# Performance work log

Measured on AMD Instinct MI355X. Metric: run time of the kernel, lower is better.

## Reference

```python
import jax, jax.numpy as jnp
import numpy as np

NH, NL, NP = 8, 4, 4  # heads, levels, points per head per level
SHAPES = [(100, 134), (50, 67), (25, 34), (13, 17)]  # (H, W) per level, strides 8/16/32/64


def rms_norm(x, w, eps=1e-6):
    return x * jax.lax.rsqrt(jnp.mean(x * x, axis=-1, keepdims=True) + eps) * w


def bilinear_sample(value_l, loc, H, W):
    """grid_sample(bilinear, zeros padding, align_corners=False) equivalent.
    value_l: (bs, nh, H*W, d); loc: (bs, Lq, nh, P, 2) normalized to [0,1].
    Returns (bs, Lq, nh, P, d)."""
    bs, Lq, nh, P, _ = loc.shape
    x = loc[..., 0] * W - 0.5
    y = loc[..., 1] * H - 0.5
    x0 = jnp.floor(x); y0 = jnp.floor(y)
    lx = x - x0; ly = y - y0
    x0i = x0.astype(jnp.int32); y0i = y0.astype(jnp.int32)
    out = None
    for dy, dx in ((0, 0), (0, 1), (1, 0), (1, 1)):
        wgt = (lx if dx else 1.0 - lx) * (ly if dy else 1.0 - ly)
        xi = x0i + dx; yi = y0i + dy
        valid = (xi >= 0) & (xi < W) & (yi >= 0) & (yi < H)
        idx = jnp.clip(yi, 0, H - 1) * W + jnp.clip(xi, 0, W - 1)  # (bs,Lq,nh,P)
        idx_t = idx.transpose(0, 2, 1, 3).reshape(bs, nh, Lq * P)
        g = jnp.take_along_axis(value_l, idx_t[..., None], axis=2)  # (bs,nh,Lq*P,d)
        g = g.reshape(bs, nh, Lq, P, -1).transpose(0, 2, 1, 3, 4)    # (bs,Lq,nh,P,d)
        term = g * (wgt * valid)[..., None]
        out = term if out is None else out + term
    return out


def _forward(query, query_pos, reference_points, norm_attn_w, Wv, bv, Woff, boff, Waw, baw, Wo, bo, ls_attn_g, norm_ffn_w, W1, b1, W2, b2, W3, b3, ls_ffn_g):
    bs, Lq, C = query.shape
    d = C // NH
    # --- pre-norm MSDeformAttn with identity=0 (LayerScale residual applied outside) ---
    normed = rms_norm(query, norm_attn_w)
    q = normed + query_pos  # query_pos only affects offsets/weights, not value
    value = (normed @ Wv.T + bv).reshape(bs, Lq, NH, d).transpose(0, 2, 1, 3)  # (bs,nh,Nv,d)
    off = (q @ Woff.T + boff).reshape(bs, Lq, NH, NL, NP, 2)
    aw = jax.nn.softmax((q @ Waw.T + baw).reshape(bs, Lq, NH, NL * NP), axis=-1)
    aw = aw.reshape(bs, Lq, NH, NL, NP)
    normalizer = jnp.array([[w, h] for (h, w) in SHAPES], dtype=query.dtype)  # (NL,2) = (W,H)
    loc = reference_points[:, :, None, :, None, :] + off / normalizer[None, None, None, :, None, :]
    out = jnp.zeros((bs, Lq, NH, d), query.dtype)
    start = 0
    for l, (H, W) in enumerate(SHAPES):
        v_l = jax.lax.dynamic_slice_in_dim(value, start, H * W, axis=2)
        samp = bilinear_sample(v_l, loc[:, :, :, l], H, W)  # (bs,Lq,nh,P,d)
        out = out + jnp.einsum('bqhpd,bqhp->bqhd', samp, aw[:, :, :, l])
        start += H * W
    attn_out = out.reshape(bs, Lq, C) @ Wo.T + bo
    x = query + ls_attn_g * attn_out
    # --- pre-norm SwiGLU FFN with LayerScale residual ---
    n2 = rms_norm(x, norm_ffn_w)
    h = jax.nn.silu(n2 @ W1.T + b1) * (n2 @ W2.T + b2)
    return x + ls_ffn_g * (h @ W3.T + b3)


def setup_inputs() -> dict:
    key = jax.random.key(0)
    ks = jax.random.split(key, 12)
    bs, C, dffn = 2, 256, 1024
    Lq = sum(h * w for h, w in SHAPES)  # 17821
    p = 0.02
    return {
        'query': jax.random.normal(ks[0], (bs, Lq, C), jnp.float32),
        'query_pos': jax.random.normal(ks[1], (bs, Lq, C), jnp.float32),
        'reference_points': jax.random.uniform(ks[2], (bs, Lq, NL, 2), jnp.float32),
        'spatial_shapes': jnp.array(SHAPES, jnp.int32),
        'level_start_index': jnp.array(np.cumsum([0] + [h * w for h, w in SHAPES])[:-1], jnp.int32),
        'norm_attn_w': jnp.ones((C,), jnp.float32),
        'Wv': jax.random.normal(ks[3], (C, C), jnp.float32) * p,
        'bv': jnp.zeros((C,), jnp.float32),
        'Woff': jax.random.normal(ks[4], (NH * NL * NP * 2, C), jnp.float32) * p,
        'boff': jax.random.uniform(ks[5], (NH * NL * NP * 2,), jnp.float32, -1.0, 1.0),
        'Waw': jax.random.normal(ks[6], (NH * NL * NP, C), jnp.float32) * p,
        'baw': jnp.zeros((NH * NL * NP,), jnp.float32),
        'Wo': jax.random.normal(ks[7], (C, C), jnp.float32) * p,
        'bo': jnp.zeros((C,), jnp.float32),
        'ls_attn_g': jnp.full((C,), 1e-4, jnp.float32),
        'norm_ffn_w': jnp.ones((C,), jnp.float32),
        'W1': jax.random.normal(ks[8], (dffn, C), jnp.float32) * p,
        'b1': jnp.zeros((dffn,), jnp.float32),
        'W2': jax.random.normal(ks[9], (dffn, C), jnp.float32) * p,
        'b2': jnp.zeros((dffn,), jnp.float32),
        'W3': jax.random.normal(ks[10], (C, dffn), jnp.float32) * p,
        'b3': jnp.zeros((C,), jnp.float32),
        'ls_ffn_g': jnp.full((C,), 1e-4, jnp.float32),
    }


def reference(query, query_pos, reference_points, spatial_shapes, level_start_index, norm_attn_w, Wv, bv, Woff, boff, Waw, baw, Wo, bo, ls_attn_g, norm_ffn_w, W1, b1, W2, b2, W3, b3, ls_ffn_g):
    del spatial_shapes, level_start_index  # static shapes baked into SHAPES
    return _forward(query, query_pos, reference_points, norm_attn_w, Wv, bv, Woff, boff, Waw, baw, Wo, bo, ls_attn_g, norm_ffn_w, W1, b1, W2, b2, W3, b3, ls_ffn_g)
```

## Files before the change

### kernel.cpp

```cpp
#include <hip/hip_runtime.h>
#include <hip/hip_bf16.h>
#include <cstddef>

#define LQ   17821
#define BS   2
#define MTOK (BS * LQ)
#define CDIM 256
#define NHD  8
#define DHEAD 32
#define DFFN 1024

typedef short bf16x4 __attribute__((ext_vector_type(4)));
typedef short bf16x8 __attribute__((ext_vector_type(8)));
typedef float f32x4  __attribute__((ext_vector_type(4)));
typedef float f32x2  __attribute__((ext_vector_type(2)));

__device__ __forceinline__ unsigned char fp8_enc(float f) {
#if __has_builtin(__builtin_amdgcn_cvt_pk_fp8_f32)
    return (unsigned char)(__builtin_amdgcn_cvt_pk_fp8_f32(f, f, 0, false) & 0xff);
#else
    unsigned s = (__float_as_uint(f) >> 31) << 7;
    float af = fabsf(f);
    if (af < 0.0078125f) return (unsigned char)s;
    af = fminf(af, 448.f);
    unsigned b = __float_as_uint(af);
    int e = (int)(b >> 23) - 127 + 7;
    unsigned m = (b >> 20) & 7;
    if (b & 0x80000) { m++; if (m == 8) { m = 0; e++; } }
    if (e < 1) return (unsigned char)s;
    if (e > 15) { e = 15; m = 6; }
    return (unsigned char)(s | ((unsigned)e << 3) | m);
#endif
}

__device__ __forceinline__ float fp8_dec_byte(unsigned x) {
    unsigned s = (x >> 7) & 1, e = (x >> 3) & 15, m = x & 7;
    float v = e ? __uint_as_float(((e + 120u) << 23) | (m << 20))
                : (float)m * 0.001953125f;
    return s ? -v : v;
}

template <bool HI>
__device__ __forceinline__ f32x2 fp8_dec2(unsigned d) {
#if __has_builtin(__builtin_amdgcn_cvt_pk_f32_fp8)
    return __builtin_amdgcn_cvt_pk_f32_fp8(d, HI);
#else
    f32x2 r;
    r[0] = fp8_dec_byte((d >> (HI ? 16 : 0)) & 0xff);
    r[1] = fp8_dec_byte((d >> (HI ? 24 : 8)) & 0xff);
    return r;
#endif
}

struct CastJobs {
    const float* src[7];
    __hip_bfloat16* dst[7];
    const float* colw[7];
    int n[7];
};

__global__ __launch_bounds__(256)
void cast_all(CastJobs j) {
    const int seg = blockIdx.y;
    const int i = blockIdx.x * 256 + threadIdx.x;
    if (i < j.n[seg]) {
        float v = j.src[seg][i];
        if (j.colw[seg]) v *= j.colw[seg][i & 255];
        j.dst[seg][i] = (__hip_bfloat16)v;
    }
}

__device__ __forceinline__ ushort bfpack(float f) {
    __hip_bfloat16 h = (__hip_bfloat16)f;
    return *(ushort*)&h;
}

template <bool ADD_POS>
__global__ __launch_bounds__(256)
void rmsnorm_kernel(const float* __restrict__ x, const float* __restrict__ pos,
                    const float* __restrict__ w,
                    __hip_bfloat16* __restrict__ outN, __hip_bfloat16* __restrict__ outQ) {
    const int tok = blockIdx.x * 4 + (threadIdx.x >> 6);
    if (tok >= MTOK) return;
    const int lane = threadIdx.x & 63;
    const size_t base = (size_t)tok * CDIM + lane * 4;
    const float4 v = *(const float4*)&x[base];
    float ss = v.x * v.x + v.y * v.y + v.z * v.z + v.w * v.w;
#pragma unroll
    for (int m = 1; m < 64; m <<= 1) ss += __shfl_xor(ss, m, 64);
    const float r = rsqrtf(ss * (1.0f / CDIM) + 1e-6f);
    const float4 wv = *(const float4*)&w[lane * 4];
    const float n0 = v.x * r * wv.x, n1 = v.y * r * wv.y;
    const float n2 = v.z * r * wv.z, n3 = v.w * r * wv.w;
    ushort4 o;
    o.x = bfpack(n0); o.y = bfpack(n1); o.z = bfpack(n2); o.w = bfpack(n3);
    *(ushort4*)&outN[base] = o;
    if (ADD_POS) {
        const float4 p = *(const float4*)&pos[base];
        ushort4 q;
        q.x = bfpack(n0 + p.x); q.y = bfpack(n1 + p.y);
        q.z = bfpack(n2 + p.z); q.w = bfpack(n3 + p.w);
        *(ushort4*)&outQ[base] = q;
    }
}

__global__ __launch_bounds__(256)
void rowrms_kernel(const __hip_bfloat16* __restrict__ x, float* __restrict__ r) {
    const int tok = blockIdx.x * 4 + (threadIdx.x >> 6);
    if (tok >= MTOK) return;
    const int lane = threadIdx.x & 63;
    const ushort4 u = *(const ushort4*)&x[(size_t)tok * CDIM + lane * 4];
    const float v0 = __uint_as_float((unsigned)u.x << 16);
    const float v1 = __uint_as_float((unsigned)u.y << 16);
    const float v2 = __uint_as_float((unsigned)u.z << 16);
    const float v3 = __uint_as_float((unsigned)u.w << 16);
    float ss = v0 * v0 + v1 * v1 + v2 * v2 + v3 * v3;
#pragma unroll
    for (int m = 1; m < 64; m <<= 1) ss += __shfl_xor(ss, m, 64);
    if (lane == 0) r[tok] = rsqrtf(ss * (1.0f / CDIM) + 1e-6f);
}

#define GBM 128
#define GBN 128

template <int MODE, int BKT, typename OUTT>
__global__ __launch_bounds__(256, 2)
void mfma_gemm(const __hip_bfloat16* __restrict__ A,
               const __hip_bfloat16* __restrict__ B1, const float* __restrict__ bias1,
               const float* __restrict__ bias2,
               const float* __restrict__ resid, const __hip_bfloat16* __restrict__ residb,
               const float* __restrict__ ls,
               OUTT* __restrict__ out, int M, int N, int K) {
    constexpr int LDKT = BKT + 8;
    constexpr int CH = BKT / 16;
    constexpr int CPR = BKT / 8;

    __shared__ short As[GBM * LDKT];
    __shared__ short Bs[GBN * LDKT];

    const int tid = threadIdx.x;
    const int m0 = blockIdx.x * GBM;
    const int n0 = blockIdx.y * GBN;
    const int wave = tid >> 6;
    const int lane = tid & 63;
    const int wm = (wave >> 1) * 64;
    const int wn = (wave & 1) * 64;
    const int fr = lane & 15;
    const int fq = lane >> 4;

    f32x4 acc[4][4] = {};

    int srow[CH], skc[CH];
#pragma unroll
    for (int cc = 0; cc < CH; ++cc) {
        const int g = tid + cc * 256;
        srow[cc] = g / CPR;
        skc[cc] = (g % CPR) * 8;
    }
    const uint4 zero4 = make_uint4(0, 0, 0, 0);

    uint4 ra[CH], rb[CH];
#pragma unroll
    for (int cc = 0; cc < CH; ++cc) {
        const int gm = m0 + srow[cc];
        ra[cc] = (gm < M) ? *(const uint4*)&A[(size_t)gm * K + skc[cc]] : zero4;
        rb[cc] = *(const uint4*)&B1[(size_t)(n0 + srow[cc]) * K + skc[cc]];
    }

    for (int k0 = 0; k0 < K; k0 += BKT) {
        __syncthreads();
#pragma unroll
        for (int cc = 0; cc < CH; ++cc) {
            short* pa = &As[srow[cc] * LDKT + skc[cc]];
            short* pb = &Bs[srow[cc] * LDKT + skc[cc]];
            union { uint4 u; bf16x4 h[2]; } cv;
            cv.u = ra[cc]; ((bf16x4*)pa)[0] = cv.h[0]; ((bf16x4*)pa)[1] = cv.h[1];
            cv.u = rb[cc]; ((bf16x4*)pb)[0] = cv.h[0]; ((bf16x4*)pb)[1] = cv.h[1];
        }
        __syncthreads();

        if (k0 + BKT < K) {
            const int kn = k0 + BKT;
#pragma unroll
            for (int cc = 0; cc < CH; ++cc) {
                const int gm = m0 + srow[cc];
                ra[cc] = (gm < M) ? *(const uint4*)&A[(size_t)gm * K + kn + skc[cc]] : zero4;
                rb[cc] = *(const uint4*)&B1[(size_t)(n0 + srow[cc]) * K + kn + skc[cc]];
            }
        }

#pragma unroll
        for (int kk = 0; kk < BKT; kk += 32) {
            const int kq = kk + fq * 8;
            bf16x8 af[4], bfr[4];
#pragma unroll
            for (int i = 0; i < 4; ++i)
                af[i] = *(const bf16x8*)&As[(wm + i * 16 + fr) * LDKT + kq];
#pragma unroll
            for (int j = 0; j < 4; ++j)
                bfr[j] = *(const bf16x8*)&Bs[(wn + j * 16 + fr) * LDKT + kq];
#pragma unroll
            for (int i = 0; i < 4; ++i)
#pragma unroll
                for (int j = 0; j < 4; ++j)
                    acc[i][j] = __builtin_amdgcn_mfma_f32_16x16x32_bf16(af[i], bfr[j], acc[i][j], 0, 0, 0);
        }
    }

#pragma unroll
    for (int i = 0; i < 4; ++i) {
#pragma unroll
        for (int r = 0; r < 4; ++r) {
            const int m = m0 + wm + i * 16 + fq * 4 + r;
            if (m >= M) continue;
#pragma unroll
            for (int j = 0; j < 4; ++j) {
                const int n = n0 + wn + j * 16 + fr;
                float v;
                if constexpr (MODE == 4)
                    v = acc[i][j][r] + ((n < 256) ? bias1[n] : bias2[n - 256]);
                else
                    v = acc[i][j][r] + bias1[n];
                if constexpr (MODE == 0 || MODE == 4) {
                    out[(size_t)m * N + n] = (OUTT)v;
                } else if constexpr (MODE == 1) {
                    const int b = (m >= LQ) ? 1 : 0;
                    const int qi = m - b * LQ;
                    const int h = n >> 5;
                    const int c = n & 31;
                    ((unsigned char*)out)[((size_t)(b * NHD + h) * LQ + qi) * DHEAD + c] = fp8_enc(v);
                } else if constexpr (MODE == 2) {
                    out[(size_t)m * N + n] =
                        (OUTT)(resid[(size_t)m * N + n] + ls[n] * v);
                } else {
                    const float rx = __uint_as_float(
                        (unsigned)(*(const ushort*)&residb[(size_t)m * N + n]) << 16);
                    out[(size_t)m * N + n] = (OUTT)(rx + ls[n] * v);
                }
            }
        }
    }
}

__global__ __launch_bounds__(256, 3)
void mfma_swiglu(const __hip_bfloat16* __restrict__ A,
                 const __hip_bfloat16* __restrict__ B1, const float* __restrict__ bias1,
                 const __hip_bfloat16* __restrict__ B2, const float* __restrict__ bias2,
                 const float* __restrict__ rrow,
                 __hip_bfloat16* __restrict__ out, int M) {
    constexpr int BKT = 32, LDKT = 40, K = CDIM, N = DFFN;
    __shared__ short As[128 * LDKT];
    __shared__ short Bs[64 * LDKT];
    __shared__ short Bs2[64 * LDKT];

    const int tid = threadIdx.x;
    const int m0 = blockIdx.x * 128;
    const int n0 = blockIdx.y * 64;
    const int wave = tid >> 6;
    const int lane = tid & 63;
    const int wm = (wave >> 1) * 64;
    const int wn = (wave & 1) * 32;
    const int fr = lane & 15;
    const int fq = lane >> 4;

    f32x4 acc[4][2] = {};
    f32x4 acc2[4][2] = {};

    const int arow = tid >> 2;
    const int akc = (tid & 3) * 8;
    const uint4 zero4 = make_uint4(0, 0, 0, 0);

    uint4 ra0, ra1, rb, rc;
    {
        const int gm0 = m0 + arow, gm1 = m0 + arow + 64;
        ra0 = (gm0 < M) ? *(const uint4*)&A[(size_t)gm0 * K + akc] : zero4;
        ra1 = (gm1 < M) ? *(const uint4*)&A[(size_t)gm1 * K + akc] : zero4;
        rb = *(const uint4*)&B1[(size_t)(n0 + arow) * K + akc];
        rc = *(const uint4*)&B2[(size_t)(n0 + arow) * K + akc];
    }

    for (int k0 = 0; k0 < K; k0 += BKT) {
        __syncthreads();
        {
            union { uint4 u; bf16x4 h[2]; } cv;
            short* pa0 = &As[arow * LDKT + akc];
            short* pa1 = &As[(arow + 64) * LDKT + akc];
            short* pb = &Bs[arow * LDKT + akc];
            short* pc = &Bs2[arow * LDKT + akc];
            cv.u = ra0; ((bf16x4*)pa0)[0] = cv.h[0]; ((bf16x4*)pa0)[1] = cv.h[1];
            cv.u = ra1; ((bf16x4*)pa1)[0] = cv.h[0]; ((bf16x4*)pa1)[1] = cv.h[1];
            cv.u = rb;  ((bf16x4*)pb)[0] = cv.h[0]; ((bf16x4*)pb)[1] = cv.h[1];
            cv.u = rc;  ((bf16x4*)pc)[0] = cv.h[0]; ((bf16x4*)pc)[1] = cv.h[1];
        }
        __syncthreads();

        if (k0 + BKT < K) {
            const int kn = k0 + BKT + akc;
            const int gm0 = m0 + arow, gm1 = m0 + arow + 64;
            ra0 = (gm0 < M) ? *(const uint4*)&A[(size_t)gm0 * K + kn] : zero4;
            ra1 = (gm1 < M) ? *(const uint4*)&A[(size_t)gm1 * K + kn] : zero4;
            rb = *(const uint4*)&B1[(size_t)(n0 + arow) * K + kn];
            rc = *(const uint4*)&B2[(size_t)(n0 + arow) * K + kn];
        }

        const int kq = fq * 8;
        bf16x8 af[4], bfr[2], bg[2];
#pragma unroll
        for (int i = 0; i < 4; ++i)
            af[i] = *(const bf16x8*)&As[(wm + i * 16 + fr) * LDKT + kq];
#pragma unroll
        for (int j = 0; j < 2; ++j) {
            bfr[j] = *(const bf16x8*)&Bs[(wn + j * 16 + fr) * LDKT + kq];
            bg[j] = *(const bf16x8*)&Bs2[(wn + j * 16 + fr) * LDKT + kq];
        }
#pragma unroll
        for (int i = 0; i < 4; ++i)
#pragma unroll
            for (int j = 0; j < 2; ++j) {
                acc[i][j] = __builtin_amdgcn_mfma_f32_16x16x32_bf16(af[i], bfr[j], acc[i][j], 0, 0, 0);
                acc2[i][j] = __builtin_amdgcn_mfma_f32_16x16x32_bf16(af[i], bg[j], acc2[i][j], 0, 0, 0);
            }
    }

#pragma unroll
    for (int i = 0; i < 4; ++i) {
#pragma unroll
        for (int r = 0; r < 4; ++r) {
            const int m = m0 + wm + i * 16 + fq * 4 + r;
            if (m >= M) continue;
            const float rm = rrow[m];
#pragma unroll
            for (int j = 0; j < 2; ++j) {
                const int n = n0 + wn + j * 16 + fr;
                const float v1 = acc[i][j][r] * rm + bias1[n];
                const float v2 = acc2[i][j][r] * rm + bias2[n];
                const float sig = 1.0f / (1.0f + expf(-v1));
                out[(size_t)m * N + n] = (__hip_bfloat16)(v1 * sig * v2);
            }
        }
    }
}

__global__ __launch_bounds__(256)
void sample_kernel(const unsigned char* __restrict__ value,
                   const ushort* __restrict__ proj,
                   const float* __restrict__ ref,
                   __hip_bfloat16* __restrict__ out) {
    __shared__ float wsm[4][NHD][16];
    __shared__ int2  sTap[4][64][9];

    const int tok0 = blockIdx.x * 4;
    const int t = threadIdx.x;

    if (t < 32) {
        const int tl = t >> 3, h = t & 7;
        const int row = tok0 + tl;
        if (row < MTOK) {
            const ushort* lg = &proj[(size_t)row * 384 + 256 + h * 16];
            float v[16];
            float mx = -3.4e38f;
#pragma unroll
            for (int i = 0; i < 16; ++i) {
                v[i] = __uint_as_float((unsigned)lg[i] << 16);
                mx = fmaxf(mx, v[i]);
            }
            float s = 0.f;
#pragma unroll
            for (int i = 0; i < 16; ++i) { v[i] = expf(v[i] - mx); s += v[i]; }
            const float inv = 1.0f / s;
#pragma unroll
            for (int i = 0; i < 16; ++i) wsm[tl][h][i] = v[i] * inv;
        }
    }
    __syncthreads();

#pragma unroll
    for (int e = t; e < 512; e += 256) {
        const int tl = e >> 7, hp = e & 127;
        const int row = tok0 + tl;
        if (row < MTOK) {
            const int h = hp >> 4, pt = hp & 15, lv = pt >> 2;
            const int Hs[4] = {100, 50, 25, 13};
            const int Ws[4] = {134, 67, 34, 17};
            const int stt[4] = {0, 13400, 16750, 17600};
            const int H = Hs[lv], W = Ws[lv];
            const float rx = ref[((size_t)row * 4 + lv) * 2 + 0];
            const float ry = ref[((size_t)row * 4 + lv) * 2 + 1];
            const float ox = __uint_as_float((unsigned)proj[(size_t)row * 384 + h * 32 + pt * 2 + 0] << 16);
            const float oy = __uint_as_float((unsigned)proj[(size_t)row * 384 + h * 32 + pt * 2 + 1] << 16);
            const float xf = rx * (float)W + ox - 0.5f;
            const float yf = ry * (float)H + oy - 0.5f;
            const float x0f = floorf(xf), y0f = floorf(yf);
            const float fx = xf - x0f, fy = yf - y0f;
            const int x0 = (int)x0f, y0 = (int)y0f;
            const float aw = wsm[tl][h][pt];
            const int b = (row >= LQ) ? 1 : 0;
            const int base = (b * NHD + h) * LQ + stt[lv];
#pragma unroll
            for (int tap = 0; tap < 4; ++tap) {
                const int dy = tap >> 1, dx = tap & 1;
                const int xi = x0 + dx, yi = y0 + dy;
                const bool valid = (xi >= 0) & (xi < W) & (yi >= 0) & (yi < H);
                const float wgt = (dx ? fx : 1.f - fx) * (dy ? fy : 1.f - fy) * aw;
                sTap[tl][pt * 4 + tap][h] = valid
                    ? make_int2((base + yi * W + xi) * DHEAD, __float_as_int(wgt))
                    : make_int2(0, 0);
            }
        }
    }
    __syncthreads();

    const int tl = t >> 6, lane = t & 63;
    const int row = tok0 + tl;
    if (row >= MTOK) return;
    const int h = lane >> 3, c0 = (lane & 7) * 4;
    const unsigned char* vb = value + c0;
    float a0 = 0.f, a1 = 0.f, a2 = 0.f, a3 = 0.f;
#pragma unroll 8
    for (int i = 0; i < 64; ++i) {
        const int2 tp = sTap[tl][i][h];
        const float w = __int_as_float(tp.y);
        const unsigned d = *(const unsigned*)(vb + (size_t)tp.x);
        const f32x2 lo = fp8_dec2<false>(d);
        const f32x2 hi = fp8_dec2<true>(d);
        a0 = fmaf(w, lo[0], a0);
        a1 = fmaf(w, lo[1], a1);
        a2 = fmaf(w, hi[0], a2);
        a3 = fmaf(w, hi[1], a3);
    }
    ushort4 o;
    o.x = bfpack(a0); o.y = bfpack(a1); o.z = bfpack(a2); o.w = bfpack(a3);
    *(ushort4*)&out[(size_t)row * 256 + h * 32 + c0] = o;
}

extern "C" void kernel_launch(void* const* d_in, const int* in_sizes, int n_in,
                              void* d_out, int out_size, void* d_ws, size_t ws_size,
                              hipStream_t stream) {
    const float* query      = (const float*)d_in[0];
    const float* query_pos  = (const float*)d_in[1];
    const float* ref        = (const float*)d_in[2];
    const float* norm_attn_w = (const float*)d_in[5];
    const float* Wv   = (const float*)d_in[6];
    const float* bv   = (const float*)d_in[7];
    const float* Woff = (const float*)d_in[8];
    const float* boff = (const float*)d_in[9];
    const float* Waw  = (const float*)d_in[10];
    const float* baw  = (const float*)d_in[11];
    const float* Wo   = (const float*)d_in[12];
    const float* bo   = (const float*)d_in[13];
    const float* ls_attn = (const float*)d_in[14];
    const float* norm_ffn_w = (const float*)d_in[15];
    const float* W1 = (const float*)d_in[16];
    const float* b1 = (const float*)d_in[17];
    const float* W2 = (const float*)d_in[18];
    const float* b2 = (const float*)d_in[19];
    const float* W3 = (const float*)d_in[20];
    const float* b3 = (const float*)d_in[21];
    const float* ls_ffn = (const float*)d_in[22];
    float* out = (float*)d_out;

    char* ws = (char*)d_ws;
    const size_t MCb = (size_t)MTOK * CDIM * 2;

    __hip_bfloat16* normed_bf  = (__hip_bfloat16*)(ws);
    __hip_bfloat16* q_bf       = (__hip_bfloat16*)(ws + MCb);
    unsigned char*  value_u8   = (unsigned char*)(ws + 2 * MCb);
    __hip_bfloat16* proj_bf    = (__hip_bfloat16*)(ws + 3 * MCb);
    __hip_bfloat16* sampled_bf = (__hip_bfloat16*)(ws);
    __hip_bfloat16* x_bf       = (__hip_bfloat16*)(ws + MCb);
    float*          r_f        = (float*)(ws + 2 * MCb);
    __hip_bfloat16* h_bf       = (__hip_bfloat16*)(ws + 3 * MCb);
    __hip_bfloat16* wbf        = (__hip_bfloat16*)(ws + 7 * MCb);

    __hip_bfloat16* Wv_bf    = wbf;
    __hip_bfloat16* Wproj_bf = wbf + 65536;
    __hip_bfloat16* Wo_bf    = wbf + 163840;
    __hip_bfloat16* W1_bf    = wbf + 229376;
    __hip_bfloat16* W2_bf    = wbf + 491520;
    __hip_bfloat16* W3_bf    = wbf + 753664;

    CastJobs cj;
    cj.src[0] = Wv;   cj.dst[0] = Wv_bf;            cj.colw[0] = nullptr; cj.n[0] = 65536;
    cj.src[1] = Woff; cj.dst[1] = Wproj_bf;         cj.colw[1] = nullptr; cj.n[1] = 65536;
    cj.src[2] = Waw;  cj.dst[2] = Wproj_bf + 65536; cj.colw[2] = nullptr; cj.n[2] = 32768;
    cj.src[3] = Wo;   cj.dst[3] = Wo_bf;            cj.colw[3] = nullptr; cj.n[3] = 65536;
    cj.src[4] = W1;   cj.dst[4] = W1_bf;            cj.colw[4] = norm_ffn_w; cj.n[4] = 262144;
    cj.src[5] = W2;   cj.dst[5] = W2_bf;            cj.colw[5] = norm_ffn_w; cj.n[5] = 262144;
    cj.src[6] = W3;   cj.dst[6] = W3_bf;            cj.colw[6] = nullptr; cj.n[6] = 262144;
    cast_all<<<dim3(1024, 7), 256, 0, stream>>>(cj);

    const int gx = (MTOK + GBM - 1) / GBM;
    const int gr = (MTOK + 3) / 4;

    rmsnorm_kernel<true><<<gr, 256, 0, stream>>>(query, query_pos, norm_attn_w, normed_bf, q_bf);
    mfma_gemm<1, 64, unsigned char><<<dim3(gx, 2), 256, 0, stream>>>(
        normed_bf, Wv_bf, bv, nullptr, nullptr, nullptr, nullptr, value_u8, MTOK, CDIM, CDIM);
    mfma_gemm<4, 64, __hip_bfloat16><<<dim3(gx, 3), 256, 0, stream>>>(
        q_bf, Wproj_bf, boff, baw, nullptr, nullptr, nullptr, proj_bf, MTOK, 384, CDIM);
    sample_kernel<<<gr, 256, 0, stream>>>(value_u8, (const ushort*)proj_bf, ref, sampled_bf);
    mfma_gemm<2, 64, __hip_bfloat16><<<dim3(gx, 2), 256, 0, stream>>>(
        sampled_bf, Wo_bf, bo, nullptr, query, nullptr, ls_attn, x_bf, MTOK, CDIM, CDIM);
    rowrms_kernel<<<gr, 256, 0, stream>>>(x_bf, r_f);
    mfma_swiglu<<<dim3(gx, DFFN / 64), 256, 0, stream>>>(
        x_bf, W1_bf, b1, W2_bf, b2, r_f, h_bf, MTOK);
    mfma_gemm<5, 64, float><<<dim3(gx, 2), 256, 0, stream>>>(
        h_bf, W3_bf, b3, nullptr, nullptr, x_bf, ls_ffn, out, MTOK, CDIM, DFFN);
}
```

Before: 407.2 us.

## Store SwiGLU hidden activations as FP8 and swizzle GEMM grids for N-tile locality

The SwiGLU kernel now writes its 1024-wide hidden activation in FP8 instead of bf16. The final W3 GEMM gets an A8 path that loads those FP8 bytes and decodes them to bf16 while staging into shared memory, which halves the traffic of the largest intermediate tensor. Every GEMM launch also moves to a 1D grid where consecutive blocks share an M tile across the N tiles, so the A rows are reused in cache. The cost is extra precision loss in the FFN hidden state and some decode ALU work during staging.

```diff
diff --git a/kernel.cpp b/kernel.cpp
--- a/kernel.cpp
+++ b/kernel.cpp
@@ -52,6 +52,23 @@
 #endif
 }
 
+__device__ __forceinline__ ushort bfpack(float f) {
+    __hip_bfloat16 h = (__hip_bfloat16)f;
+    return *(ushort*)&h;
+}
+
+__device__ __forceinline__ void stage_a8(short* p, uint2 d) {
+    const f32x2 p0 = fp8_dec2<false>(d.x), p1 = fp8_dec2<true>(d.x);
+    const f32x2 p2 = fp8_dec2<false>(d.y), p3 = fp8_dec2<true>(d.y);
+    bf16x4 lo, hi;
+    lo[0] = (short)bfpack(p0[0]); lo[1] = (short)bfpack(p0[1]);
+    lo[2] = (short)bfpack(p1[0]); lo[3] = (short)bfpack(p1[1]);
+    hi[0] = (short)bfpack(p2[0]); hi[1] = (short)bfpack(p2[1]);
+    hi[2] = (short)bfpack(p3[0]); hi[3] = (short)bfpack(p3[1]);
+    ((bf16x4*)p)[0] = lo;
+    ((bf16x4*)p)[1] = hi;
+}
+
 struct CastJobs {
     const float* src[7];
     __hip_bfloat16* dst[7];
@@ -68,11 +85,6 @@
         if (j.colw[seg]) v *= j.colw[seg][i & 255];
         j.dst[seg][i] = (__hip_bfloat16)v;
     }
-}
-
-__device__ __forceinline__ ushort bfpack(float f) {
-    __hip_bfloat16 h = (__hip_bfloat16)f;
-    return *(ushort*)&h;
 }
 
 template <bool ADD_POS>
@@ -123,14 +135,14 @@
 #define GBM 128
 #define GBN 128
 
-template <int MODE, int BKT, typename OUTT>
+template <int MODE, int BKT, typename OUTT, bool A8 = false>
 __global__ __launch_bounds__(256, 2)
-void mfma_gemm(const __hip_bfloat16* __restrict__ A,
+void mfma_gemm(const void* __restrict__ Av,
                const __hip_bfloat16* __restrict__ B1, const float* __restrict__ bias1,
                const float* __restrict__ bias2,
                const float* __restrict__ resid, const __hip_bfloat16* __restrict__ residb,
                const float* __restrict__ ls,
-               OUTT* __restrict__ out, int M, int N, int K) {
+               OUTT* __restrict__ out, int M, int N, int K, int nsw) {
     constexpr int LDKT = BKT + 8;
     constexpr int CH = BKT / 16;
     constexpr int CPR = BKT / 8;
@@ -138,9 +150,13 @@
     __shared__ short As[GBM * LDKT];
     __shared__ short Bs[GBN * LDKT];
 
+    const __hip_bfloat16* A = (const __hip_bfloat16*)Av;
+    const unsigned char* A8p = (const unsigned char*)Av;
+
     const int tid = threadIdx.x;
-    const int m0 = blockIdx.x * GBM;
-    const int n0 = blockIdx.y * GBN;
+    const int bid = blockIdx.x;
+    const int m0 = (bid / nsw) * GBM;
+    const int n0 = (bid % nsw) * GBN;
     const int wave = tid >> 6;
     const int lane = tid & 63;
     const int wm = (wave >> 1) * 64;
@@ -158,12 +174,17 @@
         skc[cc] = (g % CPR) * 8;
     }
     const uint4 zero4 = make_uint4(0, 0, 0, 0);
+    const uint2 zero2 = make_uint2(0, 0);
 
     uint4 ra[CH], rb[CH];
+    uint2 ra8[A8 ? CH : 1];
 #pragma unroll
     for (int cc = 0; cc < CH; ++cc) {
         const int gm = m0 + srow[cc];
-        ra[cc] = (gm < M) ? *(const uint4*)&A[(size_t)gm * K + skc[cc]] : zero4;
+        if constexpr (A8)
+            ra8[cc] = (gm < M) ? *(const uint2*)&A8p[(size_t)gm * K + skc[cc]] : zero2;
+        else
+            ra[cc] = (gm < M) ? *(const uint4*)&A[(size_t)gm * K + skc[cc]] : zero4;
         rb[cc] = *(const uint4*)&B1[(size_t)(n0 + srow[cc]) * K + skc[cc]];
     }
 
@@ -173,8 +194,13 @@
         for (int cc = 0; cc < CH; ++cc) {
             short* pa = &As[srow[cc] * LDKT + skc[cc]];
             short* pb = &Bs[srow[cc] * LDKT + skc[cc]];
+            if constexpr (A8) {
+                stage_a8(pa, ra8[cc]);
+            } else {
+                union { uint4 u; bf16x4 h[2]; } cv;
+                cv.u = ra[cc]; ((bf16x4*)pa)[0] = cv.h[0]; ((bf16x4*)pa)[1] = cv.h[1];
+            }
             union { uint4 u; bf16x4 h[2]; } cv;
-            cv.u = ra[cc]; ((bf16x4*)pa)[0] = cv.h[0]; ((bf16x4*)pa)[1] = cv.h[1];
             cv.u = rb[cc]; ((bf16x4*)pb)[0] = cv.h[0]; ((bf16x4*)pb)[1] = cv.h[1];
         }
         __syncthreads();
@@ -184,7 +210,10 @@
 #pragma unroll
             for (int cc = 0; cc < CH; ++cc) {
                 const int gm = m0 + srow[cc];
-                ra[cc] = (gm < M) ? *(const uint4*)&A[(size_t)gm * K + kn + skc[cc]] : zero4;
+                if constexpr (A8)
+                    ra8[cc] = (gm < M) ? *(const uint2*)&A8p[(size_t)gm * K + kn + skc[cc]] : zero2;
+                else
+                    ra[cc] = (gm < M) ? *(const uint4*)&A[(size_t)gm * K + kn + skc[cc]] : zero4;
                 rb[cc] = *(const uint4*)&B1[(size_t)(n0 + srow[cc]) * K + kn + skc[cc]];
             }
         }
@@ -247,15 +276,16 @@
                  const __hip_bfloat16* __restrict__ B1, const float* __restrict__ bias1,
                  const __hip_bfloat16* __restrict__ B2, const float* __restrict__ bias2,
                  const float* __restrict__ rrow,
-                 __hip_bfloat16* __restrict__ out, int M) {
+                 unsigned char* __restrict__ out, int M) {
     constexpr int BKT = 32, LDKT = 40, K = CDIM, N = DFFN;
     __shared__ short As[128 * LDKT];
     __shared__ short Bs[64 * LDKT];
     __shared__ short Bs2[64 * LDKT];
 
     const int tid = threadIdx.x;
-    const int m0 = blockIdx.x * 128;
-    const int n0 = blockIdx.y * 64;
+    const int bid = blockIdx.x;
+    const int m0 = (bid >> 4) * 128;
+    const int n0 = (bid & 15) * 64;
     const int wave = tid >> 6;
     const int lane = tid & 63;
     const int wm = (wave >> 1) * 64;
@@ -335,7 +365,7 @@
                 const float v1 = acc[i][j][r] * rm + bias1[n];
                 const float v2 = acc2[i][j][r] * rm + bias2[n];
                 const float sig = 1.0f / (1.0f + expf(-v1));
-                out[(size_t)m * N + n] = (__hip_bfloat16)(v1 * sig * v2);
+                out[(size_t)m * N + n] = fp8_enc(v1 * sig * v2);
             }
         }
     }
@@ -469,7 +499,7 @@
     __hip_bfloat16* sampled_bf = (__hip_bfloat16*)(ws);
     __hip_bfloat16* x_bf       = (__hip_bfloat16*)(ws + MCb);
     float*          r_f        = (float*)(ws + 2 * MCb);
-    __hip_bfloat16* h_bf       = (__hip_bfloat16*)(ws + 3 * MCb);
+    unsigned char*  h_u8       = (unsigned char*)(ws + 3 * MCb);
     __hip_bfloat16* wbf        = (__hip_bfloat16*)(ws + 7 * MCb);
 
     __hip_bfloat16* Wv_bf    = wbf;
@@ -493,16 +523,16 @@
     const int gr = (MTOK + 3) / 4;
 
     rmsnorm_kernel<true><<<gr, 256, 0, stream>>>(query, query_pos, norm_attn_w, normed_bf, q_bf);
-    mfma_gemm<1, 64, unsigned char><<<dim3(gx, 2), 256, 0, stream>>>(
-        normed_bf, Wv_bf, bv, nullptr, nullptr, nullptr, nullptr, value_u8, MTOK, CDIM, CDIM);
-    mfma_gemm<4, 64, __hip_bfloat16><<<dim3(gx, 3), 256, 0, stream>>>(
-        q_bf, Wproj_bf, boff, baw, nullptr, nullptr, nullptr, proj_bf, MTOK, 384, CDIM);
+    mfma_gemm<1, 64, unsigned char><<<gx * 2, 256, 0, stream>>>(
+        normed_bf, Wv_bf, bv, nullptr, nullptr, nullptr, nullptr, value_u8, MTOK, CDIM, CDIM, 2);
+    mfma_gemm<4, 64, __hip_bfloat16><<<gx * 3, 256, 0, stream>>>(
+        q_bf, Wproj_bf, boff, baw, nullptr, nullptr, nullptr, proj_bf, MTOK, 384, CDIM, 3);
     sample_kernel<<<gr, 256, 0, stream>>>(value_u8, (const ushort*)proj_bf, ref, sampled_bf);
-    mfma_gemm<2, 64, __hip_bfloat16><<<dim3(gx, 2), 256, 0, stream>>>(
-        sampled_bf, Wo_bf, bo, nullptr, query, nullptr, ls_attn, x_bf, MTOK, CDIM, CDIM);
+    mfma_gemm<2, 64, __hip_bfloat16><<<gx * 2, 256, 0, stream>>>(
+        sampled_bf, Wo_bf, bo, nullptr, query, nullptr, ls_attn, x_bf, MTOK, CDIM, CDIM, 2);
     rowrms_kernel<<<gr, 256, 0, stream>>>(x_bf, r_f);
-    mfma_swiglu<<<dim3(gx, DFFN / 64), 256, 0, stream>>>(
-        x_bf, W1_bf, b1, W2_bf, b2, r_f, h_bf, MTOK);
-    mfma_gemm<5, 64, float><<<dim3(gx, 2), 256, 0, stream>>>(
-        h_bf, W3_bf, b3, nullptr, nullptr, x_bf, ls_ffn, out, MTOK, CDIM, DFFN);
-}
+    mfma_swiglu<<<gx * 16, 256, 0, stream>>>(
+        x_bf, W1_bf, b1, W2_bf, b2, r_f, h_u8, MTOK);
+    mfma_gemm<5, 64, float, true><<<gx * 2, 256, 0, stream>>>(
+        h_u8, W3_bf, b3, nullptr, nullptr, x_bf, ls_ffn, out, MTOK, CDIM, DFFN, 2);
+}
```

Result: faster. 385.4 us (-5.4%).
